# Performance work log

Hardware: AMD Instinct MI355X
Metric: run time of the kernel (lower is better)

The kernel has to match this reference:

```python
import jax, jax.numpy as jnp
import numpy as np

N = 100000
E = 1600000
E_OUT = 400000
IN_DIM = 16
HID = 64
OUT_DIM = 2
L = 6
BN_EPS = 1e-5


def setup_inputs() -> dict:
    key = jax.random.key(0)
    ks = jax.random.split(key, 12)
    x = jax.random.normal(ks[0], (N, IN_DIM), dtype=jnp.float32)
    edge_index = jax.random.randint(ks[1], (2, E), 0, N, dtype=jnp.int64)
    edge_index_out = jax.random.randint(ks[2], (2, E_OUT), 0, N, dtype=jnp.int64)
    s_emb = 1.0 / np.sqrt(IN_DIM)
    s_hid = 1.0 / np.sqrt(HID)
    W_emb = jax.random.uniform(ks[3], (IN_DIM, HID), jnp.float32, -s_emb, s_emb)
    b_emb = jax.random.uniform(ks[4], (HID,), jnp.float32, -s_emb, s_emb)
    conv_W = jax.random.uniform(ks[5], (L, HID, HID), jnp.float32, -s_hid, s_hid)
    conv_b = jnp.zeros((L, HID), jnp.float32)
    bn_gamma = jnp.ones((L, HID), jnp.float32)
    bn_beta = jnp.zeros((L, HID), jnp.float32)
    s_fc = 1.0 / np.sqrt(2 * HID)
    fc_W = jax.random.uniform(ks[6], (2 * HID, OUT_DIM), jnp.float32, -s_fc, s_fc)
    fc_b = jax.random.uniform(ks[7], (OUT_DIM,), jnp.float32, -s_fc, s_fc)
    return dict(x=x, edge_index=edge_index, edge_index_out=edge_index_out,
                W_emb=W_emb, b_emb=b_emb, conv_W=conv_W, conv_b=conv_b,
                bn_gamma=bn_gamma, bn_beta=bn_beta, fc_W=fc_W, fc_b=fc_b)


def gcn_conv(h, W, b, src, dst, norm):
    # PyG GCNConv: h' = scatter_add(norm * (hW)[src] -> dst) + b
    hw = h @ W                                   # [N, HID]
    msgs = hw[src] * norm[:, None]               # [E+N, HID] gather
    agg = jax.ops.segment_sum(msgs, dst, num_segments=N)
    return agg + b


def batchnorm_train(h, gamma, beta):
    mean = jnp.mean(h, axis=0)
    var = jnp.mean(jnp.square(h - mean), axis=0)  # biased var (BN training)
    return (h - mean) * jax.lax.rsqrt(var + BN_EPS) * gamma + beta


def reference(x, edge_index, edge_index_out, W_emb, b_emb, conv_W, conv_b,
              bn_gamma, bn_beta, fc_W, fc_b):
    # add self-loops + symmetric normalization (computed once, shared by layers)
    loop = jnp.arange(N, dtype=edge_index.dtype)
    src = jnp.concatenate([edge_index[0], loop])
    dst = jnp.concatenate([edge_index[1], loop])
    deg = jax.ops.segment_sum(jnp.ones_like(dst, dtype=jnp.float32), dst, num_segments=N)
    dinv = jnp.where(deg > 0, jax.lax.rsqrt(jnp.maximum(deg, 1.0)), 0.0)
    norm = dinv[src] * dinv[dst]

    x_embed = x @ W_emb + b_emb                  # node embedding [N, HID]
    for i in range(L):
        h = gcn_conv(x_embed, conv_W[i], conv_b[i], src, dst, norm)
        h = jax.nn.relu(batchnorm_train(h, bn_gamma[i], bn_beta[i]))
        x_embed = x_embed + h                    # residual

    e_src, e_dst = edge_index_out[0], edge_index_out[1]
    edge_repr = jnp.concatenate([x_embed[e_src], x_embed[e_dst]], axis=-1)  # [E_out, 2*HID]
    return edge_repr @ fc_W + fc_b
```

## Files before the change

### kernel.cpp

```cpp
#include <hip/hip_runtime.h>

#define NN 100000
#define NE 1600000
#define NEO 400000
#define HID 64
#define NL 6
#define BN_EPS 1e-5f

#define SPMM_BLOCKS 6250
#define SCAN_BS 512
#define SCAN_NB 196
#define GRP_ROWS 12500

#define BIN_CHUNK 2048
#define BIN_BLOCKS ((NE + BIN_CHUNK - 1) / BIN_CHUNK)
#define BIN_CAP 210000
#define B2_BPG 98

#define OFF_ECOL 0
#define OFF_XE   NE
#define OFF_AGG  (OFF_XE + NN * 32)
#define OFF_HWB  (OFF_AGG + NN * 32)

#define OD_DINV   0
#define OD_ROWPTR 100352
#define OD_CC     200704
#define OD_BSUM   300704
#define OD_SS     300960
#define OD_SUMS   301088
#define OD_GCUR   309280

typedef __attribute__((ext_vector_type(8))) short bf16x8;
typedef __attribute__((ext_vector_type(4))) float f32x4;

static __device__ __forceinline__ unsigned short f2bf(float f) {
    unsigned u = __float_as_uint(f);
    unsigned r = (u + 0x7FFF + ((u >> 16) & 1)) >> 16;
    return (unsigned short)r;
}
static __device__ __forceinline__ float bflo(unsigned u) {
    return __uint_as_float(u << 16);
}
static __device__ __forceinline__ float bfhi(unsigned u) {
    return __uint_as_float(u & 0xFFFF0000u);
}

__global__ void k_bin(const int* __restrict__ src, const int* __restrict__ dst,
                      int* __restrict__ cnt, int* __restrict__ gcur,
                      int* __restrict__ bsrc, int* __restrict__ bdst) {
    __shared__ int cnt8[8], base8[8], off8[8];
    int t = threadIdx.x;
    if (t < 8) { cnt8[t] = 0; off8[t] = 0; }
    __syncthreads();
    int cb = blockIdx.x * BIN_CHUNK;
    int s[8], d[8], g[8];
#pragma unroll
    for (int j = 0; j < 8; j++) {
        int e = cb + t + j * 256;
        s[j] = (e < NE) ? src[e] : -1;
        d[j] = (e < NE) ? dst[e] : -1;
        if (d[j] >= 0) {
            g[j] = (unsigned)d[j] / GRP_ROWS;
            atomicAdd(&cnt8[g[j]], 1);
            atomicAdd(&cnt[d[j]], 1);
        }
    }
    __syncthreads();
    if (t < 8) base8[t] = t * BIN_CAP + atomicAdd(&gcur[t], cnt8[t]);
    __syncthreads();
#pragma unroll
    for (int j = 0; j < 8; j++) {
        if (d[j] >= 0) {
            int pos = base8[g[j]] + atomicAdd(&off8[g[j]], 1);
            bsrc[pos] = s[j];
            bdst[pos] = d[j];
        }
    }
}

__global__ void k_scanA(const int* __restrict__ cnt, int* __restrict__ rowptr,
                        int* __restrict__ bsum, float* __restrict__ dinv) {
    __shared__ int sh[SCAN_BS];
    int t = threadIdx.x;
    int i = blockIdx.x * SCAN_BS + t;
    int v = (i < NN) ? cnt[i] : 0;
    sh[t] = v;
    __syncthreads();
    for (int off = 1; off < SCAN_BS; off <<= 1) {
        int a = (t >= off) ? sh[t - off] : 0;
        __syncthreads();
        sh[t] += a;
        __syncthreads();
    }
    if (i < NN) {
        rowptr[i] = sh[t] - v;
        dinv[i] = rsqrtf((float)(v + 1));
    }
    if (t == SCAN_BS - 1) bsum[blockIdx.x] = sh[t];
}

__global__ void k_scanB(int* __restrict__ bsum) {
    __shared__ int sh[256];
    int t = threadIdx.x;
    int v = (t < SCAN_NB) ? bsum[t] : 0;
    sh[t] = v;
    __syncthreads();
    for (int off = 1; off < 256; off <<= 1) {
        int a = (t >= off) ? sh[t - off] : 0;
        __syncthreads();
        sh[t] += a;
        __syncthreads();
    }
    if (t < SCAN_NB) bsum[t] = (t == 0) ? 0 : sh[t - 1];
}

__global__ void k_scanC(int* __restrict__ rowptr, const int* __restrict__ bsum,
                        int* __restrict__ cursor) {
    int i = blockIdx.x * SCAN_BS + threadIdx.x;
    if (i < NN) {
        int rp = rowptr[i] + bsum[blockIdx.x];
        rowptr[i] = rp;
        cursor[i] = rp;
    }
    if (i == 0) rowptr[NN] = NE;
}

__global__ void k_build2(const int* __restrict__ gcur, const int* __restrict__ bsrc,
                         const int* __restrict__ bdst, int* __restrict__ cursor,
                         int* __restrict__ ecol) {
    int g = blockIdx.x & 7;
    int b = blockIdx.x >> 3;
    int n = gcur[g];
    int base = g * BIN_CAP;
    for (int i = b * blockDim.x + threadIdx.x; i < n; i += B2_BPG * blockDim.x) {
        int d = bdst[base + i];
        int s = bsrc[base + i];
        int pos = atomicAdd(&cursor[d], 1);
        ecol[pos] = s;
    }
}

__global__ void k_embed(const float* __restrict__ x, const float* __restrict__ W,
                        const float* __restrict__ b, unsigned short* __restrict__ xe16) {
    __shared__ float Ws[16 * 64];
    __shared__ float bs[64];
    int t = threadIdx.x;
    for (int i = t; i < 16 * 64; i += 256) Ws[i] = W[i];
    if (t < 64) bs[t] = b[t];
    __syncthreads();
    int c = t & 63, r = t >> 6;
    int n0 = blockIdx.x * 64;
    for (int n = n0 + r; n < n0 + 64 && n < NN; n += 4) {
        const float* xr = x + n * 16;
        float acc = bs[c];
#pragma unroll
        for (int k = 0; k < 16; k++) acc = fmaf(xr[k], Ws[k * 64 + c], acc);
        xe16[(size_t)n * 64 + c] = f2bf(acc);
    }
}

__global__ void k_hw(unsigned short* __restrict__ xe16,
                     const float* __restrict__ W, const float* __restrict__ dinv,
                     const unsigned short* __restrict__ agg16,
                     const float* __restrict__ gamma, const float* __restrict__ beta,
                     const double* __restrict__ sumsPrev, double* __restrict__ sumsCur,
                     unsigned short* __restrict__ hwb, int apply) {
    __shared__ unsigned short Wt[64 * 72];
    __shared__ unsigned short Xb[64 * 72];
    __shared__ float sss[128];
    int t = threadIdx.x;
    int n0 = blockIdx.x * 64;
    if (blockIdx.x == 0) {
        for (int i = t; i < 2048; i += 256) sumsCur[i] = 0.0;
    }
    if (apply && t < 64) {
        double s = 0.0, q = 0.0;
#pragma unroll
        for (int k = 0; k < 16; k++) {
            s += sumsPrev[k * 128 + t];
            q += sumsPrev[k * 128 + 64 + t];
        }
        double mean = s / (double)NN;
        double var = q / (double)NN - mean * mean;
        float sc = gamma[t] * rsqrtf((float)var + BN_EPS);
        sss[t] = sc;
        sss[64 + t] = beta[t] - (float)mean * sc;
    }

    {
        int c = t & 63, r = t >> 6;
#pragma unroll
        for (int jj = 0; jj < 4; jj++) {
            float w0 = W[(r * 16 + jj * 4 + 0) * 64 + c];
            float w1 = W[(r * 16 + jj * 4 + 1) * 64 + c];
            float w2 = W[(r * 16 + jj * 4 + 2) * 64 + c];
            float w3 = W[(r * 16 + jj * 4 + 3) * 64 + c];
            uint2 pk;
            pk.x = ((unsigned)f2bf(w1) << 16) | f2bf(w0);
            pk.y = ((unsigned)f2bf(w3) << 16) | f2bf(w2);
            *(uint2*)&Wt[c * 72 + r * 16 + jj * 4] = pk;
        }
    }
    __syncthreads();

    {
        int n = t >> 2, kq = t & 3;
        int node = n0 + n;
        unsigned xs[8] = {0, 0, 0, 0, 0, 0, 0, 0};
        if (node < NN) {
            const uint4* xr = (const uint4*)(xe16 + (size_t)node * 64 + kq * 16);
            uint4 x0 = xr[0], x1 = xr[1];
            xs[0] = x0.x; xs[1] = x0.y; xs[2] = x0.z; xs[3] = x0.w;
            xs[4] = x1.x; xs[5] = x1.y; xs[6] = x1.z; xs[7] = x1.w;
            if (apply) {
                const uint4* ar = (const uint4*)(agg16 + (size_t)node * 64 + kq * 16);
                uint4 a0 = ar[0], a1 = ar[1];
                unsigned as[8] = {a0.x, a0.y, a0.z, a0.w, a1.x, a1.y, a1.z, a1.w};
                int c = kq * 16;
#pragma unroll
                for (int i = 0; i < 8; i++) {
                    float v0 = bflo(xs[i]) +
                               fmaxf(fmaf(bflo(as[i]), sss[c + 2 * i], sss[64 + c + 2 * i]), 0.f);
                    float v1 = bfhi(xs[i]) +
                               fmaxf(fmaf(bfhi(as[i]), sss[c + 2 * i + 1], sss[64 + c + 2 * i + 1]), 0.f);
                    xs[i] = ((unsigned)f2bf(v1) << 16) | f2bf(v0);
                }
                uint4* xw = (uint4*)(xe16 + (size_t)node * 64 + kq * 16);
                xw[0] = make_uint4(xs[0], xs[1], xs[2], xs[3]);
                xw[1] = make_uint4(xs[4], xs[5], xs[6], xs[7]);
            }
        }
        *(uint4*)&Xb[n * 72 + kq * 16] = make_uint4(xs[0], xs[1], xs[2], xs[3]);
        *(uint4*)&Xb[n * 72 + kq * 16 + 8] = make_uint4(xs[4], xs[5], xs[6], xs[7]);
    }
    __syncthreads();

    int lane = t & 63, w = t >> 6;
    int m = lane & 15, quad = lane >> 4;
    f32x4 acc[4];
#pragma unroll
    for (int tc = 0; tc < 4; tc++) acc[tc] = (f32x4){0.f, 0.f, 0.f, 0.f};
#pragma unroll
    for (int s = 0; s < 2; s++) {
        bf16x8 bfr = *(const bf16x8*)&Xb[(w * 16 + m) * 72 + s * 32 + quad * 8];
#pragma unroll
        for (int tc = 0; tc < 4; tc++) {
            bf16x8 afr = *(const bf16x8*)&Wt[(tc * 16 + m) * 72 + s * 32 + quad * 8];
            acc[tc] = __builtin_amdgcn_mfma_f32_16x16x32_bf16(afr, bfr, acc[tc], 0, 0, 0);
        }
    }
    int node = n0 + w * 16 + m;
    if (node < NN) {
        float di = dinv[node];
#pragma unroll
        for (int tc = 0; tc < 4; tc++) {
            int c0 = tc * 16 + quad * 4;
            uint2 pk;
            pk.x = ((unsigned)f2bf(acc[tc][1] * di) << 16) | f2bf(acc[tc][0] * di);
            pk.y = ((unsigned)f2bf(acc[tc][3] * di) << 16) | f2bf(acc[tc][2] * di);
            *(uint2*)(hwb + (size_t)node * 64 + c0) = pk;
        }
    }
}

__global__ void k_spmm(const int* __restrict__ rowptr, const int* __restrict__ ecol,
                       const unsigned short* __restrict__ hwb, const float* __restrict__ dinv,
                       unsigned short* __restrict__ agg16, double* __restrict__ sums) {
    int t = threadIdx.x;
    int w = t >> 6, l = t & 63;
    int r = l >> 4;
    int sub = (l >> 3) & 1;
    int q = l & 7;
    const uint4* hw4 = (const uint4*)hwb;
    float ls[8], lq[8];
#pragma unroll
    for (int j = 0; j < 8; j++) { ls[j] = 0.f; lq[j] = 0.f; }
    for (int row0 = blockIdx.x * 16 + w * 4; row0 < NN; row0 += SPMM_BLOCKS * 16) {
        int row = row0 + r;
        bool valid = row < NN;
        int p0 = 0, p1 = 0;
        float a[8];
#pragma unroll
        for (int j = 0; j < 8; j++) a[j] = 0.f;
        if (valid) {
            p0 = rowptr[row];
            p1 = rowptr[row + 1];
            if (sub == 0) {
                uint4 sv = hw4[(size_t)row * 8 + q];
                a[0] = bflo(sv.x); a[1] = bfhi(sv.x); a[2] = bflo(sv.y); a[3] = bfhi(sv.y);
                a[4] = bflo(sv.z); a[5] = bfhi(sv.z); a[6] = bflo(sv.w); a[7] = bfhi(sv.w);
            }
        }
        int p = p0 + sub;
        for (; p + 2 < p1; p += 4) {
            int s0 = ecol[p], s1 = ecol[p + 2];
            uint4 u0 = hw4[(size_t)s0 * 8 + q];
            uint4 u1 = hw4[(size_t)s1 * 8 + q];
            a[0] += bflo(u0.x); a[1] += bfhi(u0.x); a[2] += bflo(u0.y); a[3] += bfhi(u0.y);
            a[4] += bflo(u0.z); a[5] += bfhi(u0.z); a[6] += bflo(u0.w); a[7] += bfhi(u0.w);
            a[0] += bflo(u1.x); a[1] += bfhi(u1.x); a[2] += bflo(u1.y); a[3] += bfhi(u1.y);
            a[4] += bflo(u1.z); a[5] += bfhi(u1.z); a[6] += bflo(u1.w); a[7] += bfhi(u1.w);
        }
        if (p < p1) {
            int s0 = ecol[p];
            uint4 u0 = hw4[(size_t)s0 * 8 + q];
            a[0] += bflo(u0.x); a[1] += bfhi(u0.x); a[2] += bflo(u0.y); a[3] += bfhi(u0.y);
            a[4] += bflo(u0.z); a[5] += bfhi(u0.z); a[6] += bflo(u0.w); a[7] += bfhi(u0.w);
        }
#pragma unroll
        for (int j = 0; j < 8; j++) a[j] += __shfl_xor(a[j], 8, 64);
        if (valid && sub == 0) {
            float di = dinv[row];
            unsigned pk[4];
#pragma unroll
            for (int j = 0; j < 4; j++) {
                float v0 = a[2 * j] * di, v1 = a[2 * j + 1] * di;
                pk[j] = ((unsigned)f2bf(v1) << 16) | f2bf(v0);
            }
            *(uint4*)(agg16 + (size_t)row * 64 + 8 * q) = make_uint4(pk[0], pk[1], pk[2], pk[3]);
#pragma unroll
            for (int j = 0; j < 4; j++) {
                float v0 = bflo(pk[j]), v1 = bfhi(pk[j]);
                ls[2 * j] += v0; ls[2 * j + 1] += v1;
                lq[2 * j] = fmaf(v0, v0, lq[2 * j]);
                lq[2 * j + 1] = fmaf(v1, v1, lq[2 * j + 1]);
            }
        }
    }
#pragma unroll
    for (int j = 0; j < 8; j++) {
        ls[j] += __shfl_xor(ls[j], 16, 64); ls[j] += __shfl_xor(ls[j], 32, 64);
        lq[j] += __shfl_xor(lq[j], 16, 64); lq[j] += __shfl_xor(lq[j], 32, 64);
    }
    __shared__ float Ss[4][64], Sq[4][64];
    if (l < 8) {
#pragma unroll
        for (int j = 0; j < 8; j++) {
            Ss[w][8 * l + j] = ls[j];
            Sq[w][8 * l + j] = lq[j];
        }
    }
    __syncthreads();
    if (t < 64) {
        float a = Ss[0][t] + Ss[1][t] + Ss[2][t] + Ss[3][t];
        float b = Sq[0][t] + Sq[1][t] + Sq[2][t] + Sq[3][t];
        double* sh = sums + (blockIdx.x & 15) * 128;
        atomicAdd(&sh[t], (double)a);
        atomicAdd(&sh[64 + t], (double)b);
    }
}

__global__ void k_finalize(const double* __restrict__ sums, const float* __restrict__ gamma,
                           const float* __restrict__ beta, float* __restrict__ ss) {
    int c = threadIdx.x;
    double s = 0.0, q = 0.0;
#pragma unroll
    for (int k = 0; k < 16; k++) { s += sums[k * 128 + c]; q += sums[k * 128 + 64 + c]; }
    double mean = s / (double)NN;
    double var = q / (double)NN - mean * mean;
    float sc = gamma[c] * rsqrtf((float)var + BN_EPS);
    ss[c] = sc;
    ss[64 + c] = beta[c] - (float)mean * sc;
}

__global__ void k_apply(const unsigned short* __restrict__ agg16, const float* __restrict__ ss,
                        unsigned short* __restrict__ xe16) {
    int i = blockIdx.x * blockDim.x + threadIdx.x;
    if (i < NN * 8) {
        int c0 = (i & 7) * 8;
        uint4 av = *(const uint4*)(agg16 + (size_t)i * 8);
        uint4 xv = *(const uint4*)(xe16 + (size_t)i * 8);
        unsigned as[4] = {av.x, av.y, av.z, av.w};
        unsigned xs[4] = {xv.x, xv.y, xv.z, xv.w};
#pragma unroll
        for (int j = 0; j < 4; j++) {
            int c = c0 + 2 * j;
            float v0 = bflo(xs[j]) + fmaxf(fmaf(bflo(as[j]), ss[c], ss[64 + c]), 0.f);
            float v1 = bfhi(xs[j]) + fmaxf(fmaf(bfhi(as[j]), ss[c + 1], ss[64 + c + 1]), 0.f);
            xs[j] = ((unsigned)f2bf(v1) << 16) | f2bf(v0);
        }
        *(uint4*)(xe16 + (size_t)i * 8) = make_uint4(xs[0], xs[1], xs[2], xs[3]);
    }
}

__global__ void k_out(const int* __restrict__ esrc, const int* __restrict__ edst,
                      const unsigned short* __restrict__ xe16, const float* __restrict__ fcW,
                      const float* __restrict__ fcb, float* __restrict__ out) {
    __shared__ float Ws[256];
    __shared__ float bs[2];
    int t = threadIdx.x;
    for (int i = t; i < 256; i += 256) Ws[i] = fcW[i];
    if (t < 2) bs[t] = fcb[t];
    __syncthreads();
    int e = blockIdx.x * blockDim.x + t;
    if (e < NEO) {
        int s = esrc[e], d = edst[e];
        const uint4* rs = (const uint4*)(xe16 + (size_t)s * 64);
        const uint4* rd = (const uint4*)(xe16 + (size_t)d * 64);
        float a0 = bs[0], a1 = bs[1];
#pragma unroll
        for (int i = 0; i < 8; i++) {
            uint4 v = rs[i];
            int c = i * 8;
            a0 += bflo(v.x) * Ws[(c + 0) * 2] + bfhi(v.x) * Ws[(c + 1) * 2] +
                  bflo(v.y) * Ws[(c + 2) * 2] + bfhi(v.y) * Ws[(c + 3) * 2] +
                  bflo(v.z) * Ws[(c + 4) * 2] + bfhi(v.z) * Ws[(c + 5) * 2] +
                  bflo(v.w) * Ws[(c + 6) * 2] + bfhi(v.w) * Ws[(c + 7) * 2];
            a1 += bflo(v.x) * Ws[(c + 0) * 2 + 1] + bfhi(v.x) * Ws[(c + 1) * 2 + 1] +
                  bflo(v.y) * Ws[(c + 2) * 2 + 1] + bfhi(v.y) * Ws[(c + 3) * 2 + 1] +
                  bflo(v.z) * Ws[(c + 4) * 2 + 1] + bfhi(v.z) * Ws[(c + 5) * 2 + 1] +
                  bflo(v.w) * Ws[(c + 6) * 2 + 1] + bfhi(v.w) * Ws[(c + 7) * 2 + 1];
        }
#pragma unroll
        for (int i = 0; i < 8; i++) {
            uint4 v = rd[i];
            int c = 64 + i * 8;
            a0 += bflo(v.x) * Ws[(c + 0) * 2] + bfhi(v.x) * Ws[(c + 1) * 2] +
                  bflo(v.y) * Ws[(c + 2) * 2] + bfhi(v.y) * Ws[(c + 3) * 2] +
                  bflo(v.z) * Ws[(c + 4) * 2] + bfhi(v.z) * Ws[(c + 5) * 2] +
                  bflo(v.w) * Ws[(c + 6) * 2] + bfhi(v.w) * Ws[(c + 7) * 2];
            a1 += bflo(v.x) * Ws[(c + 0) * 2 + 1] + bfhi(v.x) * Ws[(c + 1) * 2 + 1] +
                  bflo(v.y) * Ws[(c + 2) * 2 + 1] + bfhi(v.y) * Ws[(c + 3) * 2 + 1] +
                  bflo(v.z) * Ws[(c + 4) * 2 + 1] + bfhi(v.z) * Ws[(c + 5) * 2 + 1] +
                  bflo(v.w) * Ws[(c + 6) * 2 + 1] + bfhi(v.w) * Ws[(c + 7) * 2 + 1];
        }
        out[e * 2] = a0;
        out[e * 2 + 1] = a1;
    }
}

extern "C" void kernel_launch(void* const* d_in, const int* in_sizes, int n_in,
                              void* d_out, int out_size, void* d_ws, size_t ws_size,
                              hipStream_t stream) {
    const float* x      = (const float*)d_in[0];
    const int*   ei     = (const int*)d_in[1];
    const int*   eio    = (const int*)d_in[2];
    const float* W_emb  = (const float*)d_in[3];
    const float* b_emb  = (const float*)d_in[4];
    const float* conv_W = (const float*)d_in[5];
    const float* bn_g   = (const float*)d_in[7];
    const float* bn_b   = (const float*)d_in[8];
    const float* fc_W   = (const float*)d_in[9];
    const float* fc_b   = (const float*)d_in[10];
    float* out = (float*)d_out;

    float* ws   = (float*)d_ws;
    int*   ecol = (int*)(ws + OFF_ECOL);
    unsigned short* xe16  = (unsigned short*)(ws + OFF_XE);
    unsigned short* agg16 = (unsigned short*)(ws + OFF_AGG);
    unsigned short* hwb   = (unsigned short*)(ws + OFF_HWB);
    int* bsrc = (int*)(ws + OFF_XE);
    int* bdst = (int*)(ws + OFF_AGG);

    float* od     = (float*)d_out;
    float* dinv   = od + OD_DINV;
    int*   rowptr = (int*)(od + OD_ROWPTR);
    int*   cc     = (int*)(od + OD_CC);
    int*   bsum   = (int*)(od + OD_BSUM);
    float* ss     = od + OD_SS;
    double* sums  = (double*)(od + OD_SUMS);
    int*   gcur   = (int*)(od + OD_GCUR);

    const int* src  = ei;
    const int* dst  = ei + NE;
    const int* esrc = eio;
    const int* edst = eio + NEO;

    (void)hipMemsetAsync(cc, 0, NN * sizeof(int), stream);
    (void)hipMemsetAsync(gcur, 0, 8 * sizeof(int), stream);
    k_bin<<<BIN_BLOCKS, 256, 0, stream>>>(src, dst, cc, gcur, bsrc, bdst);
    k_scanA<<<SCAN_NB, SCAN_BS, 0, stream>>>(cc, rowptr, bsum, dinv);
    k_scanB<<<1, 256, 0, stream>>>(bsum);
    k_scanC<<<SCAN_NB, SCAN_BS, 0, stream>>>(rowptr, bsum, cc);
    k_build2<<<8 * B2_BPG, 256, 0, stream>>>(gcur, bsrc, bdst, cc, ecol);

    k_embed<<<(NN + 63) / 64, 256, 0, stream>>>(x, W_emb, b_emb, xe16);

    for (int l = 0; l < NL; l++) {
        double* sumsPrev = sums + ((l + 1) & 1) * 2048;
        double* sumsCur  = sums + (l & 1) * 2048;
        k_hw<<<(NN + 63) / 64, 256, 0, stream>>>(xe16, conv_W + l * 64 * 64, dinv, agg16,
                                                 bn_g + (l ? (l - 1) * 64 : 0),
                                                 bn_b + (l ? (l - 1) * 64 : 0),
                                                 sumsPrev, sumsCur, hwb, l > 0 ? 1 : 0);
        k_spmm<<<SPMM_BLOCKS, 256, 0, stream>>>(rowptr, ecol, hwb, dinv, agg16, sumsCur);
    }
    k_finalize<<<1, 64, 0, stream>>>(sums + ((NL - 1) & 1) * 2048,
                                     bn_g + (NL - 1) * 64, bn_b + (NL - 1) * 64, ss);
    k_apply<<<(NN * 8 + 255) / 256, 256, 0, stream>>>(agg16, ss, xe16);

    k_out<<<(NEO + 255) / 256, 256, 0, stream>>>(esrc, edst, xe16, fc_W, fc_b, out);
}
```

Before: 584.9 us.

## Split hidden features into column planes for cache-friendly SpMM gathers, move degree histogram

The hw output is stored as four 16-column bf16 planes, so each SpMM pass gathers 32-byte rows from a 3.2MB plane that can stay cache-resident. The SpMM loops over the planes inside one persistent-style grid, with 8 lanes splitting the edges of a row and shuffle reductions combining them. In binning, the per-destination count atomics are moved out of k_bin into a separate k_hist2 pass over the group-sorted buckets, so those atomics hit localized addresses, and the per-wave counters reduce LDS contention. The cost is four passes over ecol and rowptr per layer and an extra kernel launch.

```diff
diff --git a/kernel.cpp b/kernel.cpp
--- a/kernel.cpp
+++ b/kernel.cpp
@@ -7,15 +7,19 @@
 #define NL 6
 #define BN_EPS 1e-5f
 
-#define SPMM_BLOCKS 6250
 #define SCAN_BS 512
 #define SCAN_NB 196
 #define GRP_ROWS 12500
 
-#define BIN_CHUNK 2048
+#define BIN_CHUNK 1024
+#define BIN_J (BIN_CHUNK / 256)
 #define BIN_BLOCKS ((NE + BIN_CHUNK - 1) / BIN_CHUNK)
 #define BIN_CAP 210000
 #define B2_BPG 98
+#define H2_BPG 98
+
+#define SPMM_BLOCKS 1536
+#define NTILES 6250
 
 #define OFF_ECOL 0
 #define OFF_XE   NE
@@ -46,36 +50,53 @@
 }
 
 __global__ void k_bin(const int* __restrict__ src, const int* __restrict__ dst,
-                      int* __restrict__ cnt, int* __restrict__ gcur,
+                      int* __restrict__ gcur,
                       int* __restrict__ bsrc, int* __restrict__ bdst) {
-    __shared__ int cnt8[8], base8[8], off8[8];
-    int t = threadIdx.x;
-    if (t < 8) { cnt8[t] = 0; off8[t] = 0; }
+    __shared__ int cw[4][8], bw[4][8], ow[4][8];
+    int t = threadIdx.x;
+    int w = t >> 6;
+    if (t < 32) { ((int*)cw)[t] = 0; ((int*)ow)[t] = 0; }
     __syncthreads();
     int cb = blockIdx.x * BIN_CHUNK;
-    int s[8], d[8], g[8];
-#pragma unroll
-    for (int j = 0; j < 8; j++) {
+    int s[BIN_J], d[BIN_J], g[BIN_J];
+#pragma unroll
+    for (int j = 0; j < BIN_J; j++) {
         int e = cb + t + j * 256;
         s[j] = (e < NE) ? src[e] : -1;
         d[j] = (e < NE) ? dst[e] : -1;
         if (d[j] >= 0) {
             g[j] = (unsigned)d[j] / GRP_ROWS;
-            atomicAdd(&cnt8[g[j]], 1);
-            atomicAdd(&cnt[d[j]], 1);
-        }
-    }
-    __syncthreads();
-    if (t < 8) base8[t] = t * BIN_CAP + atomicAdd(&gcur[t], cnt8[t]);
-    __syncthreads();
-#pragma unroll
-    for (int j = 0; j < 8; j++) {
+            atomicAdd(&cw[w][g[j]], 1);
+        }
+    }
+    __syncthreads();
+    if (t < 8) {
+        int c0 = cw[0][t], c1 = cw[1][t], c2 = cw[2][t], c3 = cw[3][t];
+        int base = t * BIN_CAP + atomicAdd(&gcur[t], c0 + c1 + c2 + c3);
+        bw[0][t] = base;
+        bw[1][t] = base + c0;
+        bw[2][t] = base + c0 + c1;
+        bw[3][t] = base + c0 + c1 + c2;
+    }
+    __syncthreads();
+#pragma unroll
+    for (int j = 0; j < BIN_J; j++) {
         if (d[j] >= 0) {
-            int pos = base8[g[j]] + atomicAdd(&off8[g[j]], 1);
+            int pos = bw[w][g[j]] + atomicAdd(&ow[w][g[j]], 1);
             bsrc[pos] = s[j];
             bdst[pos] = d[j];
         }
     }
+}
+
+__global__ void k_hist2(const int* __restrict__ gcur, const int* __restrict__ bdst,
+                        int* __restrict__ cnt) {
+    int g = blockIdx.x & 7;
+    int b = blockIdx.x >> 3;
+    int n = gcur[g];
+    int base = g * BIN_CAP;
+    for (int i = b * blockDim.x + threadIdx.x; i < n; i += H2_BPG * blockDim.x)
+        atomicAdd(&cnt[bdst[base + i]], 1);
 }
 
 __global__ void k_scanA(const int* __restrict__ cnt, int* __restrict__ rowptr,
@@ -164,7 +185,7 @@
                      const unsigned short* __restrict__ agg16,
                      const float* __restrict__ gamma, const float* __restrict__ beta,
                      const double* __restrict__ sumsPrev, double* __restrict__ sumsCur,
-                     unsigned short* __restrict__ hwb, int apply) {
+                     unsigned short* __restrict__ hwp, int apply) {
     __shared__ unsigned short Wt[64 * 72];
     __shared__ unsigned short Xb[64 * 72];
     __shared__ float sss[128];
@@ -254,90 +275,85 @@
         float di = dinv[node];
 #pragma unroll
         for (int tc = 0; tc < 4; tc++) {
-            int c0 = tc * 16 + quad * 4;
             uint2 pk;
             pk.x = ((unsigned)f2bf(acc[tc][1] * di) << 16) | f2bf(acc[tc][0] * di);
             pk.y = ((unsigned)f2bf(acc[tc][3] * di) << 16) | f2bf(acc[tc][2] * di);
-            *(uint2*)(hwb + (size_t)node * 64 + c0) = pk;
-        }
-    }
-}
-
-__global__ void k_spmm(const int* __restrict__ rowptr, const int* __restrict__ ecol,
-                       const unsigned short* __restrict__ hwb, const float* __restrict__ dinv,
-                       unsigned short* __restrict__ agg16, double* __restrict__ sums) {
+            *(uint2*)(hwp + (size_t)tc * (NN * 16) + (size_t)node * 16 + quad * 4) = pk;
+        }
+    }
+}
+
+__global__ void __launch_bounds__(256, 6)
+k_spmm(const int* __restrict__ rowptr, const int* __restrict__ ecol,
+       const unsigned short* __restrict__ hwp, const float* __restrict__ dinv,
+       unsigned short* __restrict__ agg16, double* __restrict__ sums) {
     int t = threadIdx.x;
     int w = t >> 6, l = t & 63;
     int r = l >> 4;
-    int sub = (l >> 3) & 1;
-    int q = l & 7;
-    const uint4* hw4 = (const uint4*)hwb;
-    float ls[8], lq[8];
-#pragma unroll
-    for (int j = 0; j < 8; j++) { ls[j] = 0.f; lq[j] = 0.f; }
-    for (int row0 = blockIdx.x * 16 + w * 4; row0 < NN; row0 += SPMM_BLOCKS * 16) {
-        int row = row0 + r;
-        bool valid = row < NN;
-        int p0 = 0, p1 = 0;
-        float a[8];
-#pragma unroll
-        for (int j = 0; j < 8; j++) a[j] = 0.f;
-        if (valid) {
-            p0 = rowptr[row];
-            p1 = rowptr[row + 1];
+    int sub = (l >> 1) & 7;
+    int q = l & 1;
+    __shared__ float Ss[4][64], Sq[4][64];
+#pragma unroll
+    for (int p = 0; p < 4; ++p) {
+        const uint4* pl = (const uint4*)(hwp + (size_t)p * (NN * 16));
+        float ls[8], lq[8];
+#pragma unroll
+        for (int j = 0; j < 8; j++) { ls[j] = 0.f; lq[j] = 0.f; }
+        for (int tile = blockIdx.x; tile < NTILES; tile += SPMM_BLOCKS) {
+            int row = tile * 16 + w * 4 + r;
+            int p0 = rowptr[row];
+            int p1 = rowptr[row + 1];
+            float a[8];
             if (sub == 0) {
-                uint4 sv = hw4[(size_t)row * 8 + q];
+                uint4 sv = pl[(size_t)row * 2 + q];
                 a[0] = bflo(sv.x); a[1] = bfhi(sv.x); a[2] = bflo(sv.y); a[3] = bfhi(sv.y);
                 a[4] = bflo(sv.z); a[5] = bfhi(sv.z); a[6] = bflo(sv.w); a[7] = bfhi(sv.w);
+            } else {
+#pragma unroll
+                for (int j = 0; j < 8; j++) a[j] = 0.f;
             }
-        }
-        int p = p0 + sub;
-        for (; p + 2 < p1; p += 4) {
-            int s0 = ecol[p], s1 = ecol[p + 2];
-            uint4 u0 = hw4[(size_t)s0 * 8 + q];
-            uint4 u1 = hw4[(size_t)s1 * 8 + q];
-            a[0] += bflo(u0.x); a[1] += bfhi(u0.x); a[2] += bflo(u0.y); a[3] += bfhi(u0.y);
-            a[4] += bflo(u0.z); a[5] += bfhi(u0.z); a[6] += bflo(u0.w); a[7] += bfhi(u0.w);
-            a[0] += bflo(u1.x); a[1] += bfhi(u1.x); a[2] += bflo(u1.y); a[3] += bfhi(u1.y);
-            a[4] += bflo(u1.z); a[5] += bfhi(u1.z); a[6] += bflo(u1.w); a[7] += bfhi(u1.w);
-        }
-        if (p < p1) {
-            int s0 = ecol[p];
-            uint4 u0 = hw4[(size_t)s0 * 8 + q];
-            a[0] += bflo(u0.x); a[1] += bfhi(u0.x); a[2] += bflo(u0.y); a[3] += bfhi(u0.y);
-            a[4] += bflo(u0.z); a[5] += bfhi(u0.z); a[6] += bflo(u0.w); a[7] += bfhi(u0.w);
-        }
-#pragma unroll
-        for (int j = 0; j < 8; j++) a[j] += __shfl_xor(a[j], 8, 64);
-        if (valid && sub == 0) {
-            float di = dinv[row];
-            unsigned pk[4];
-#pragma unroll
-            for (int j = 0; j < 4; j++) {
-                float v0 = a[2 * j] * di, v1 = a[2 * j + 1] * di;
-                pk[j] = ((unsigned)f2bf(v1) << 16) | f2bf(v0);
+            for (int pp = p0 + sub; pp < p1; pp += 8) {
+                int s0 = ecol[pp];
+                uint4 u0 = pl[(size_t)s0 * 2 + q];
+                a[0] += bflo(u0.x); a[1] += bfhi(u0.x); a[2] += bflo(u0.y); a[3] += bfhi(u0.y);
+                a[4] += bflo(u0.z); a[5] += bfhi(u0.z); a[6] += bflo(u0.w); a[7] += bfhi(u0.w);
             }
-            *(uint4*)(agg16 + (size_t)row * 64 + 8 * q) = make_uint4(pk[0], pk[1], pk[2], pk[3]);
-#pragma unroll
-            for (int j = 0; j < 4; j++) {
-                float v0 = bflo(pk[j]), v1 = bfhi(pk[j]);
-                ls[2 * j] += v0; ls[2 * j + 1] += v1;
-                lq[2 * j] = fmaf(v0, v0, lq[2 * j]);
-                lq[2 * j + 1] = fmaf(v1, v1, lq[2 * j + 1]);
+#pragma unroll
+            for (int j = 0; j < 8; j++) {
+                a[j] += __shfl_xor(a[j], 2, 64);
+                a[j] += __shfl_xor(a[j], 4, 64);
+                a[j] += __shfl_xor(a[j], 8, 64);
             }
-        }
-    }
-#pragma unroll
-    for (int j = 0; j < 8; j++) {
-        ls[j] += __shfl_xor(ls[j], 16, 64); ls[j] += __shfl_xor(ls[j], 32, 64);
-        lq[j] += __shfl_xor(lq[j], 16, 64); lq[j] += __shfl_xor(lq[j], 32, 64);
-    }
-    __shared__ float Ss[4][64], Sq[4][64];
-    if (l < 8) {
+            if (sub == 0) {
+                float di = dinv[row];
+                unsigned pk[4];
+#pragma unroll
+                for (int j = 0; j < 4; j++) {
+                    float v0 = a[2 * j] * di, v1 = a[2 * j + 1] * di;
+                    pk[j] = ((unsigned)f2bf(v1) << 16) | f2bf(v0);
+                }
+                *(uint4*)(agg16 + (size_t)row * 64 + p * 16 + q * 8) =
+                    make_uint4(pk[0], pk[1], pk[2], pk[3]);
+#pragma unroll
+                for (int j = 0; j < 4; j++) {
+                    float v0 = bflo(pk[j]), v1 = bfhi(pk[j]);
+                    ls[2 * j] += v0; ls[2 * j + 1] += v1;
+                    lq[2 * j] = fmaf(v0, v0, lq[2 * j]);
+                    lq[2 * j + 1] = fmaf(v1, v1, lq[2 * j + 1]);
+                }
+            }
+        }
 #pragma unroll
         for (int j = 0; j < 8; j++) {
-            Ss[w][8 * l + j] = ls[j];
-            Sq[w][8 * l + j] = lq[j];
+            ls[j] += __shfl_xor(ls[j], 16, 64); ls[j] += __shfl_xor(ls[j], 32, 64);
+            lq[j] += __shfl_xor(lq[j], 16, 64); lq[j] += __shfl_xor(lq[j], 32, 64);
+        }
+        if (l < 2) {
+#pragma unroll
+            for (int j = 0; j < 8; j++) {
+                Ss[w][p * 16 + l * 8 + j] = ls[j];
+                Sq[w][p * 16 + l * 8 + j] = lq[j];
+            }
         }
     }
     __syncthreads();
@@ -448,7 +464,7 @@
     int*   ecol = (int*)(ws + OFF_ECOL);
     unsigned short* xe16  = (unsigned short*)(ws + OFF_XE);
     unsigned short* agg16 = (unsigned short*)(ws + OFF_AGG);
-    unsigned short* hwb   = (unsigned short*)(ws + OFF_HWB);
+    unsigned short* hwp   = (unsigned short*)(ws + OFF_HWB);
     int* bsrc = (int*)(ws + OFF_XE);
     int* bdst = (int*)(ws + OFF_AGG);
 
@@ -468,7 +484,8 @@
 
     (void)hipMemsetAsync(cc, 0, NN * sizeof(int), stream);
     (void)hipMemsetAsync(gcur, 0, 8 * sizeof(int), stream);
-    k_bin<<<BIN_BLOCKS, 256, 0, stream>>>(src, dst, cc, gcur, bsrc, bdst);
+    k_bin<<<BIN_BLOCKS, 256, 0, stream>>>(src, dst, gcur, bsrc, bdst);
+    k_hist2<<<8 * H2_BPG, 256, 0, stream>>>(gcur, bdst, cc);
     k_scanA<<<SCAN_NB, SCAN_BS, 0, stream>>>(cc, rowptr, bsum, dinv);
     k_scanB<<<1, 256, 0, stream>>>(bsum);
     k_scanC<<<SCAN_NB, SCAN_BS, 0, stream>>>(rowptr, bsum, cc);
@@ -482,8 +499,8 @@
         k_hw<<<(NN + 63) / 64, 256, 0, stream>>>(xe16, conv_W + l * 64 * 64, dinv, agg16,
                                                  bn_g + (l ? (l - 1) * 64 : 0),
                                                  bn_b + (l ? (l - 1) * 64 : 0),
-                                                 sumsPrev, sumsCur, hwb, l > 0 ? 1 : 0);
-        k_spmm<<<SPMM_BLOCKS, 256, 0, stream>>>(rowptr, ecol, hwb, dinv, agg16, sumsCur);
+                                                 sumsPrev, sumsCur, hwp, l > 0 ? 1 : 0);
+        k_spmm<<<SPMM_BLOCKS, 256, 0, stream>>>(rowptr, ecol, hwp, dinv, agg16, sumsCur);
     }
     k_finalize<<<1, 64, 0, stream>>>(sums + ((NL - 1) & 1) * 2048,
                                      bn_g + (NL - 1) * 64, bn_b + (NL - 1) * 64, ss);
```

After: 768.3 us. +31.3%, slower.

## Move degree histogram out of binning into a per-group pass, with per-wave bin counters

Applied to the files above, without the earlier changes.

The per-destination degree atomics move out of the binning kernel into a new kernel that reads the already group-binned destination arrays. Each group then touches only one slice of the count array, which should improve L2 locality of the atomics. The binning kernel now keeps per-wavefront group counters to cut LDS atomic contention, and its chunk size is halved so more blocks run. This adds a kernel launch and an extra read of the binned destinations.

```diff
diff --git a/kernel.cpp b/kernel.cpp
--- a/kernel.cpp
+++ b/kernel.cpp
@@ -12,10 +12,12 @@
 #define SCAN_NB 196
 #define GRP_ROWS 12500
 
-#define BIN_CHUNK 2048
+#define BIN_CHUNK 1024
+#define BIN_J (BIN_CHUNK / 256)
 #define BIN_BLOCKS ((NE + BIN_CHUNK - 1) / BIN_CHUNK)
 #define BIN_CAP 210000
 #define B2_BPG 98
+#define H2_BPG 98
 
 #define OFF_ECOL 0
 #define OFF_XE   NE
@@ -46,36 +48,53 @@
 }
 
 __global__ void k_bin(const int* __restrict__ src, const int* __restrict__ dst,
-                      int* __restrict__ cnt, int* __restrict__ gcur,
+                      int* __restrict__ gcur,
                       int* __restrict__ bsrc, int* __restrict__ bdst) {
-    __shared__ int cnt8[8], base8[8], off8[8];
-    int t = threadIdx.x;
-    if (t < 8) { cnt8[t] = 0; off8[t] = 0; }
+    __shared__ int cw[4][8], bw[4][8], ow[4][8];
+    int t = threadIdx.x;
+    int w = t >> 6;
+    if (t < 32) { ((int*)cw)[t] = 0; ((int*)ow)[t] = 0; }
     __syncthreads();
     int cb = blockIdx.x * BIN_CHUNK;
-    int s[8], d[8], g[8];
-#pragma unroll
-    for (int j = 0; j < 8; j++) {
+    int s[BIN_J], d[BIN_J], g[BIN_J];
+#pragma unroll
+    for (int j = 0; j < BIN_J; j++) {
         int e = cb + t + j * 256;
         s[j] = (e < NE) ? src[e] : -1;
         d[j] = (e < NE) ? dst[e] : -1;
         if (d[j] >= 0) {
             g[j] = (unsigned)d[j] / GRP_ROWS;
-            atomicAdd(&cnt8[g[j]], 1);
-            atomicAdd(&cnt[d[j]], 1);
-        }
-    }
-    __syncthreads();
-    if (t < 8) base8[t] = t * BIN_CAP + atomicAdd(&gcur[t], cnt8[t]);
-    __syncthreads();
-#pragma unroll
-    for (int j = 0; j < 8; j++) {
+            atomicAdd(&cw[w][g[j]], 1);
+        }
+    }
+    __syncthreads();
+    if (t < 8) {
+        int c0 = cw[0][t], c1 = cw[1][t], c2 = cw[2][t], c3 = cw[3][t];
+        int base = t * BIN_CAP + atomicAdd(&gcur[t], c0 + c1 + c2 + c3);
+        bw[0][t] = base;
+        bw[1][t] = base + c0;
+        bw[2][t] = base + c0 + c1;
+        bw[3][t] = base + c0 + c1 + c2;
+    }
+    __syncthreads();
+#pragma unroll
+    for (int j = 0; j < BIN_J; j++) {
         if (d[j] >= 0) {
-            int pos = base8[g[j]] + atomicAdd(&off8[g[j]], 1);
+            int pos = bw[w][g[j]] + atomicAdd(&ow[w][g[j]], 1);
             bsrc[pos] = s[j];
             bdst[pos] = d[j];
         }
     }
+}
+
+__global__ void k_hist2(const int* __restrict__ gcur, const int* __restrict__ bdst,
+                        int* __restrict__ cnt) {
+    int g = blockIdx.x & 7;
+    int b = blockIdx.x >> 3;
+    int n = gcur[g];
+    int base = g * BIN_CAP;
+    for (int i = b * blockDim.x + threadIdx.x; i < n; i += H2_BPG * blockDim.x)
+        atomicAdd(&cnt[bdst[base + i]], 1);
 }
 
 __global__ void k_scanA(const int* __restrict__ cnt, int* __restrict__ rowptr,
@@ -468,7 +487,8 @@
 
     (void)hipMemsetAsync(cc, 0, NN * sizeof(int), stream);
     (void)hipMemsetAsync(gcur, 0, 8 * sizeof(int), stream);
-    k_bin<<<BIN_BLOCKS, 256, 0, stream>>>(src, dst, cc, gcur, bsrc, bdst);
+    k_bin<<<BIN_BLOCKS, 256, 0, stream>>>(src, dst, gcur, bsrc, bdst);
+    k_hist2<<<8 * H2_BPG, 256, 0, stream>>>(gcur, bdst, cc);
     k_scanA<<<SCAN_NB, SCAN_BS, 0, stream>>>(cc, rowptr, bsum, dinv);
     k_scanB<<<1, 256, 0, stream>>>(bsum);
     k_scanC<<<SCAN_NB, SCAN_BS, 0, stream>>>(rowptr, bsum, cc);
```

New measurement: 601.3 us. 2.8% more time.
